# Performance work log

Hardware: AMD Instinct MI355X
Metric: run time of the kernel (lower is better)

Reference implementation:

```python
import jax, jax.numpy as jnp
import numpy as np

N_NODES = 100000
N_EDGES = 1600000
D_IN = 64
D_OUT = 64
K_ORDERS = 4  # K+1 Chebyshev orders (K=3)


def setup_inputs() -> dict:
    key = jax.random.key(0)
    k1, k2, k3, k4, k5 = jax.random.split(key, 5)
    x = jax.random.normal(k1, (N_NODES, D_IN), dtype=jnp.float32)
    edge_index = jax.random.randint(k2, (2, N_EDGES), 0, N_NODES, dtype=jnp.int64)
    edge_attr = jax.random.uniform(k3, (N_EDGES,), dtype=jnp.float32)
    weight = jax.random.normal(k4, (K_ORDERS, D_IN, D_OUT), dtype=jnp.float32) * 0.05
    bias = jax.random.normal(k5, (D_OUT,), dtype=jnp.float32) * 0.05
    return {"x": x, "edge_index": edge_index, "edge_attr": edge_attr,
            "weight": weight, "bias": bias}


def reference(x, edge_index, edge_attr, weight, bias):
    n = x.shape[0]
    row, col = edge_index[0], edge_index[1]
    # degree = number of edges per destination node (row)
    deg = jax.ops.segment_sum(jnp.ones_like(edge_attr), row, num_segments=n)
    dinv = jnp.where(deg > 0, deg ** -0.5, 0.0)
    # negative normalized adjacency acting as rescaled Laplacian
    lap = -dinv[row] * edge_attr * dinv[col]  # [E]

    def spmm(h):  # out[row] += lap * h[col]
        return jax.ops.segment_sum(lap[:, None] * h[col], row, num_segments=n)

    k_orders = weight.shape[0]
    tx0 = x
    out = tx0 @ weight[0]
    tx1 = spmm(tx0)
    out = out + tx1 @ weight[1]
    for k in range(2, k_orders):  # small fixed K, fine to unroll
        tx2 = 2.0 * spmm(tx1) - tx0
        out = out + tx2 @ weight[k]
        tx0, tx1 = tx1, tx2
    return out + bias
```

## Files before the change

kernel.cpp:

```cpp
#include <hip/hip_runtime.h>

#define D 64
#define BLK 256

#define NBSHIFT 9
#define NODES_PER_BKT 512
#define TA 4096

typedef unsigned int uint32;
typedef __attribute__((ext_vector_type(8))) short bf16x8;
typedef __attribute__((ext_vector_type(4))) float f32x4;

__device__ inline uint32 f2bf_u(float f) {
    uint32 u = __float_as_uint(f);
    u += 0x7FFFu + ((u >> 16) & 1u);
    return u >> 16;
}

__global__ void cvt_kernel(const float* __restrict__ x, uint2* __restrict__ xb, int n4) {
    int i = blockIdx.x * BLK + threadIdx.x;
    if (i < n4) {
        float4 v = ((const float4*)x)[i];
        uint2 pack;
        pack.x = f2bf_u(v.x) | (f2bf_u(v.y) << 16);
        pack.y = f2bf_u(v.z) | (f2bf_u(v.w) << 16);
        xb[i] = pack;
    }
}

__global__ void wf_kernel(const float* __restrict__ W, uint4* __restrict__ Wf) {
    int tid = blockIdx.x * 256 + threadIdx.x;
    int l = tid & 63;
    int g = tid >> 6;
    int kh = g & 1;
    int t = (g >> 1) & 3;
    int w = g >> 3;
    int n = t * 16 + (l & 15);
    int kbase = kh * 32 + (l >> 4) * 8;
    uint32 pk[4];
    #pragma unroll
    for (int i = 0; i < 4; ++i) {
        uint32 b0 = f2bf_u(W[(size_t)w * 4096 + (size_t)(kbase + 2 * i) * 64 + n]);
        uint32 b1 = f2bf_u(W[(size_t)w * 4096 + (size_t)(kbase + 2 * i + 1) * 64 + n]);
        pk[i] = b0 | (b1 << 16);
    }
    Wf[tid] = make_uint4(pk[0], pk[1], pk[2], pk[3]);
}

__global__ void hist_kernel(const int* __restrict__ row, uint32* __restrict__ bcount, int E) {
    __shared__ uint32 h[256];
    int tid = threadIdx.x;
    h[tid] = 0;
    __syncthreads();
    int base = blockIdx.x * TA;
    int end = min(base + TA, E);
    for (int e = base + tid; e < end; e += 256)
        atomicAdd(&h[(uint32)row[e] >> NBSHIFT], 1u);
    __syncthreads();
    if (h[tid]) atomicAdd(&bcount[tid], h[tid]);
}

__global__ void scan256_kernel(const uint32* __restrict__ bcount, uint32* __restrict__ gcursor,
                               uint32* __restrict__ bbase, int E) {
    __shared__ uint32 s[256];
    int tid = threadIdx.x;
    uint32 v = bcount[tid];
    s[tid] = v;
    __syncthreads();
    for (int off = 1; off < 256; off <<= 1) {
        uint32 t = (tid >= off) ? s[tid - off] : 0u;
        __syncthreads();
        s[tid] += t;
        __syncthreads();
    }
    uint32 excl = s[tid] - v;
    gcursor[tid] = excl;
    bbase[tid] = excl;
    if (tid == 255) bbase[256] = (uint32)E;
}

__global__ void binA_kernel(const int* __restrict__ row, const int* __restrict__ col,
                            const float* __restrict__ attr,
                            uint32* __restrict__ gcursor, int2* __restrict__ binned, int E) {
    __shared__ uint32 hist[256], baseg[256], lstart[256], lcur[256];
    __shared__ int2 stage[TA];
    __shared__ unsigned char sbkt[TA];
    int tid = threadIdx.x;
    int tile = blockIdx.x * TA;
    hist[tid] = 0;
    __syncthreads();

    uint32 px[16], py[16], bk[16];
    #pragma unroll
    for (int k = 0; k < 16; ++k) {
        int e = tile + k * 256 + tid;
        bk[k] = 0xFFFFFFFFu;
        if (e < E) {
            int r = row[e], c = col[e];
            uint32 b = (uint32)r >> NBSHIFT;
            bk[k] = b;
            px[k] = ((uint32)(r & (NODES_PER_BKT - 1)) << 17) | (uint32)c;
            py[k] = __float_as_uint(attr[e]);
            atomicAdd(&hist[b], 1u);
        }
    }
    __syncthreads();
    lcur[tid] = hist[tid];
    __syncthreads();
    for (int off = 1; off < 256; off <<= 1) {
        uint32 t = (tid >= off) ? lcur[tid - off] : 0u;
        __syncthreads();
        lcur[tid] += t;
        __syncthreads();
    }
    lstart[tid] = lcur[tid] - hist[tid];
    if (hist[tid] > 0) baseg[tid] = atomicAdd(&gcursor[tid], hist[tid]);
    lcur[tid] = lstart[tid];
    __syncthreads();
    #pragma unroll
    for (int k = 0; k < 16; ++k) {
        if (bk[k] != 0xFFFFFFFFu) {
            uint32 pos = atomicAdd(&lcur[bk[k]], 1u);
            stage[pos] = make_int2((int)px[k], (int)py[k]);
            sbkt[pos] = (unsigned char)bk[k];
        }
    }
    __syncthreads();
    int cnt = min(TA, E - tile);
    for (int i = tid; i < cnt; i += 256) {
        uint32 b = sbkt[i];
        uint32 dst = baseg[b] + (uint32)i - lstart[b];
        binned[dst] = stage[i];
    }
}

__global__ void binBdeg_kernel(const int2* __restrict__ binned, const uint32* __restrict__ bbase,
                               uint32* __restrict__ rowptr, float* __restrict__ dinv,
                               int N, int E) {
    __shared__ uint32 cnt[NODES_PER_BKT];
    __shared__ uint32 ps[256];
    int b = blockIdx.x;
    int tid = threadIdx.x;
    cnt[tid] = 0;
    cnt[tid + 256] = 0;
    __syncthreads();
    uint32 start = bbase[b], end = bbase[b + 1];
    for (uint32 i = start + tid; i < end; i += 256)
        atomicAdd(&cnt[(uint32)binned[i].x >> 17], 1u);
    __syncthreads();
    uint32 c0 = cnt[2 * tid], c1 = cnt[2 * tid + 1];
    ps[tid] = c0 + c1;
    __syncthreads();
    for (int off = 1; off < 256; off <<= 1) {
        uint32 t = (tid >= off) ? ps[tid - off] : 0u;
        __syncthreads();
        ps[tid] += t;
        __syncthreads();
    }
    uint32 pexcl = ps[tid] - (c0 + c1);
    int base = b << NBSHIFT;
    int n0 = base + 2 * tid, n1 = n0 + 1;
    if (n0 < N) {
        rowptr[n0] = start + pexcl;
        dinv[n0] = c0 ? rsqrtf((float)c0) : 0.0f;
    }
    if (n1 < N) {
        rowptr[n1] = start + pexcl + c0;
        dinv[n1] = c1 ? rsqrtf((float)c1) : 0.0f;
    }
    if (b == gridDim.x - 1 && tid == 0) rowptr[N] = (uint32)E;
}

__global__ void binBsort_kernel(const int2* __restrict__ binned, const uint32* __restrict__ bbase,
                                const uint32* __restrict__ rowptr, const float* __restrict__ dinv,
                                int2* __restrict__ pairs, int N) {
    __shared__ uint32 lcur[NODES_PER_BKT];
    __shared__ float ldin[NODES_PER_BKT];
    int b = blockIdx.x;
    int tid = threadIdx.x;
    int base = b << NBSHIFT;
    uint32 start = bbase[b], end = bbase[b + 1];
    for (int t = tid; t < NODES_PER_BKT; t += 256) {
        int node = base + t;
        lcur[t] = (node < N) ? (rowptr[node] - start) : 0u;
        ldin[t] = (node < N) ? dinv[node] : 0.0f;
    }
    __syncthreads();
    for (uint32 i = start + tid; i < end; i += 256) {
        int2 rec = binned[i];
        uint32 x = (uint32)rec.x;
        uint32 rl = x >> 17;
        uint32 c = x & 0x1FFFFu;
        float lap = -ldin[rl] * __int_as_float(rec.y) * dinv[c];
        uint32 pos = atomicAdd(&lcur[rl], 1u);
        pairs[start + pos] = make_int2((int)(c << 7), __float_as_int(lap));
    }
}

__global__ void spmm8_kernel(const uint32* __restrict__ rowptr, const int2* __restrict__ pairs,
                             const char* __restrict__ hb, const uint4* __restrict__ prev,
                             uint4* __restrict__ out, float scale, int N) {
    int n = blockIdx.x * 4 + (threadIdx.x >> 6);
    if (n >= N) return;
    int lane = threadIdx.x & 63;
    int q = lane >> 3;
    int sub = lane & 7;
    int off = sub * 16;
    uint32 j = rowptr[n];
    uint32 end = rowptr[n + 1];
    float a[8];
    #pragma unroll
    for (int i = 0; i < 8; ++i) a[i] = 0.0f;

    for (; j + 16 <= end; j += 16) {
        int2 m0 = pairs[j + q];
        int2 m1 = pairs[j + 8 + q];
        uint4 h0 = *(const uint4*)(hb + (uint32)m0.x + off);
        uint4 h1 = *(const uint4*)(hb + (uint32)m1.x + off);
        float l0 = __int_as_float(m0.y);
        float l1 = __int_as_float(m1.y);
        a[0] += l0 * __uint_as_float(h0.x << 16);
        a[1] += l0 * __uint_as_float(h0.x & 0xFFFF0000u);
        a[2] += l0 * __uint_as_float(h0.y << 16);
        a[3] += l0 * __uint_as_float(h0.y & 0xFFFF0000u);
        a[4] += l0 * __uint_as_float(h0.z << 16);
        a[5] += l0 * __uint_as_float(h0.z & 0xFFFF0000u);
        a[6] += l0 * __uint_as_float(h0.w << 16);
        a[7] += l0 * __uint_as_float(h0.w & 0xFFFF0000u);
        a[0] += l1 * __uint_as_float(h1.x << 16);
        a[1] += l1 * __uint_as_float(h1.x & 0xFFFF0000u);
        a[2] += l1 * __uint_as_float(h1.y << 16);
        a[3] += l1 * __uint_as_float(h1.y & 0xFFFF0000u);
        a[4] += l1 * __uint_as_float(h1.z << 16);
        a[5] += l1 * __uint_as_float(h1.z & 0xFFFF0000u);
        a[6] += l1 * __uint_as_float(h1.w << 16);
        a[7] += l1 * __uint_as_float(h1.w & 0xFFFF0000u);
    }
    for (; j < end; j += 8) {
        uint32 idx = j + q;
        bool act = idx < end;
        uint32 ci = act ? idx : (end - 1);
        int2 m = pairs[ci];
        float l = act ? __int_as_float(m.y) : 0.0f;
        uint4 h0 = *(const uint4*)(hb + (uint32)m.x + off);
        a[0] += l * __uint_as_float(h0.x << 16);
        a[1] += l * __uint_as_float(h0.x & 0xFFFF0000u);
        a[2] += l * __uint_as_float(h0.y << 16);
        a[3] += l * __uint_as_float(h0.y & 0xFFFF0000u);
        a[4] += l * __uint_as_float(h0.z << 16);
        a[5] += l * __uint_as_float(h0.z & 0xFFFF0000u);
        a[6] += l * __uint_as_float(h0.w << 16);
        a[7] += l * __uint_as_float(h0.w & 0xFFFF0000u);
    }
    #pragma unroll
    for (int i = 0; i < 8; ++i) {
        a[i] += __shfl_xor(a[i], 8);
        a[i] += __shfl_xor(a[i], 16);
        a[i] += __shfl_xor(a[i], 32);
    }

    if (q == 0) {
        float r[8];
        #pragma unroll
        for (int i = 0; i < 8; ++i) r[i] = scale * a[i];
        size_t slot = (size_t)n * 8 + sub;
        if (prev) {
            uint4 pv = prev[slot];
            r[0] -= __uint_as_float(pv.x << 16);
            r[1] -= __uint_as_float(pv.x & 0xFFFF0000u);
            r[2] -= __uint_as_float(pv.y << 16);
            r[3] -= __uint_as_float(pv.y & 0xFFFF0000u);
            r[4] -= __uint_as_float(pv.z << 16);
            r[5] -= __uint_as_float(pv.z & 0xFFFF0000u);
            r[6] -= __uint_as_float(pv.w << 16);
            r[7] -= __uint_as_float(pv.w & 0xFFFF0000u);
        }
        uint4 pack;
        pack.x = f2bf_u(r[0]) | (f2bf_u(r[1]) << 16);
        pack.y = f2bf_u(r[2]) | (f2bf_u(r[3]) << 16);
        pack.z = f2bf_u(r[4]) | (f2bf_u(r[5]) << 16);
        pack.w = f2bf_u(r[6]) | (f2bf_u(r[7]) << 16);
        out[slot] = pack;
    }
}

__global__ void gemm_mfma(const uint4* __restrict__ h0, const uint4* __restrict__ h1,
                          const uint4* __restrict__ h2, const uint4* __restrict__ h3,
                          const uint4* __restrict__ Wf, const float* __restrict__ bias,
                          float* __restrict__ out, int N) {
    int tid = threadIdx.x;
    int wave = tid >> 6;
    int lane = tid & 63;
    int quad = lane >> 4;
    int lo = lane & 15;
    int m0 = blockIdx.x * 64 + wave * 16;
    int mrow = m0 + lo;
    int mclamp = min(mrow, N - 1);

    f32x4 acc[4] = {{0.f,0.f,0.f,0.f},{0.f,0.f,0.f,0.f},{0.f,0.f,0.f,0.f},{0.f,0.f,0.f,0.f}};
    const uint4* hs[4] = { h0, h1, h2, h3 };
    #pragma unroll
    for (int w = 0; w < 4; ++w) {
        union { uint4 u; bf16x8 v; } a0, a1;
        a0.u = hs[w][(size_t)mclamp * 8 + quad];
        a1.u = hs[w][(size_t)mclamp * 8 + 4 + quad];
        #pragma unroll
        for (int t = 0; t < 4; ++t) {
            union { uint4 u; bf16x8 v; } b0, b1;
            b0.u = Wf[(w * 8 + t * 2 + 0) * 64 + lane];
            b1.u = Wf[(w * 8 + t * 2 + 1) * 64 + lane];
            acc[t] = __builtin_amdgcn_mfma_f32_16x16x32_bf16(a0.v, b0.v, acc[t], 0, 0, 0);
            acc[t] = __builtin_amdgcn_mfma_f32_16x16x32_bf16(a1.v, b1.v, acc[t], 0, 0, 0);
        }
    }
    #pragma unroll
    for (int t = 0; t < 4; ++t) {
        int col = t * 16 + lo;
        float bv = bias[col];
        #pragma unroll
        for (int r = 0; r < 4; ++r) {
            int rowi = m0 + quad * 4 + r;
            if (rowi < N) out[(size_t)rowi * 64 + col] = acc[t][r] + bv;
        }
    }
}

extern "C" void kernel_launch(void* const* d_in, const int* in_sizes, int n_in,
                              void* d_out, int out_size, void* d_ws, size_t ws_size,
                              hipStream_t stream) {
    const float* x    = (const float*)d_in[0];
    const int*   ei   = (const int*)d_in[1];
    const float* attr = (const float*)d_in[2];
    const float* W    = (const float*)d_in[3];
    const float* bias = (const float*)d_in[4];
    float* out = (float*)d_out;

    const int N = in_sizes[0] / D;
    const int E = in_sizes[1] / 2;
    const int* row = ei;
    const int* col = ei + E;
    const int NB = (N + NODES_PER_BKT - 1) >> NBSHIFT;

    char* p = (char*)d_ws;
    int2*     pairs   = (int2*)p;                p += (size_t)E * 8;
    uint2*    xb      = (uint2*)p;               p += (size_t)N * D * 2;
    uint2*    T1      = (uint2*)p;               p += (size_t)N * D * 2;
    uint2*    T2      = (uint2*)p;               p += (size_t)N * D * 2;
    uint2*    T3      = (uint2*)p;               p += (size_t)N * D * 2;
    uint4*    Wf      = (uint4*)p;               p += 2048 * 16;
    uint32*   rowptr  = (uint32*)p;              p += (size_t)(N + 1) * 4;
    uint32*   bcount  = (uint32*)p;              p += 256 * 4;
    uint32*   gcursor = (uint32*)p;              p += 256 * 4;
    uint32*   bbase   = (uint32*)p;              p += 257 * 4;
    float*    dinv    = (float*)p;
    int2*     binned  = (int2*)T3;

    const int gSp = (N + 3) / 4;
    const int gGm = (N + 63) / 64;
    const int gTile = (E + TA - 1) / TA;
    const int gCvt = ((N * D / 4) + BLK - 1) / BLK;

    hipMemsetAsync(bcount, 0, 256 * 4, stream);
    cvt_kernel<<<gCvt, BLK, 0, stream>>>(x, xb, N * D / 4);
    wf_kernel<<<8, 256, 0, stream>>>(W, Wf);
    hist_kernel<<<gTile, 256, 0, stream>>>(row, bcount, E);
    scan256_kernel<<<1, 256, 0, stream>>>(bcount, gcursor, bbase, E);
    binA_kernel<<<gTile, 256, 0, stream>>>(row, col, attr, gcursor, binned, E);
    binBdeg_kernel<<<NB, 256, 0, stream>>>(binned, bbase, rowptr, dinv, N, E);
    binBsort_kernel<<<NB, 256, 0, stream>>>(binned, bbase, rowptr, dinv, pairs, N);

    spmm8_kernel<<<gSp, BLK, 0, stream>>>(rowptr, pairs, (const char*)xb, nullptr, (uint4*)T1, 1.0f, N);
    spmm8_kernel<<<gSp, BLK, 0, stream>>>(rowptr, pairs, (const char*)T1, (const uint4*)xb, (uint4*)T2, 2.0f, N);
    spmm8_kernel<<<gSp, BLK, 0, stream>>>(rowptr, pairs, (const char*)T2, (const uint4*)T1, (uint4*)T3, 2.0f, N);
    gemm_mfma<<<gGm, BLK, 0, stream>>>((const uint4*)xb, (const uint4*)T1, (const uint4*)T2,
                                       (const uint4*)T3, Wf, bias, out, N);
}
```

Baseline: 313.8 us.

## Process two rows per wave in SpMM with interleaved prefetched gathers

The SpMM kernel now assigns two consecutive destination rows to each wavefront. It issues the first 32 edges' index and feature loads for both rows before doing any FMAs, which raises memory-level parallelism and hides gather latency, and it prefetches the previous-order term early. Row bounds are made wave-uniform with readfirstlane and tails are handled with masked loads instead of a separate loop. The trade-offs are higher register pressure from two accumulator sets and more buffered loads, which could lower occupancy, plus half as many waves in the grid.

Result: faster. 291.6 us (-7.1%).

```diff
diff --git a/kernel.cpp b/kernel.cpp
--- a/kernel.cpp
+++ b/kernel.cpp
@@ -197,75 +197,121 @@
     }
 }
 
-__global__ void spmm8_kernel(const uint32* __restrict__ rowptr, const int2* __restrict__ pairs,
-                             const char* __restrict__ hb, const uint4* __restrict__ prev,
-                             uint4* __restrict__ out, float scale, int N) {
-    int n = blockIdx.x * 4 + (threadIdx.x >> 6);
-    if (n >= N) return;
+#define LOAD16(J, END, ESAFE, M0, M1, H0, H1)                          \
+    {                                                                  \
+        uint32 i0_ = (J) + q, i1_ = (J) + 8 + q;                       \
+        uint32 c0_ = (i0_ < (END)) ? i0_ : (ESAFE);                    \
+        uint32 c1_ = (i1_ < (END)) ? i1_ : (ESAFE);                    \
+        M0 = pairs[c0_];                                               \
+        M1 = pairs[c1_];                                               \
+        H0 = *(const uint4*)(hb + (uint32)M0.x + off);                 \
+        H1 = *(const uint4*)(hb + (uint32)M1.x + off);                 \
+    }
+
+#define FMA16(J, END, M0, M1, H0, H1, A)                               \
+    {                                                                  \
+        uint32 i0_ = (J) + q, i1_ = (J) + 8 + q;                       \
+        float l0_ = (i0_ < (END)) ? __int_as_float(M0.y) : 0.0f;       \
+        float l1_ = (i1_ < (END)) ? __int_as_float(M1.y) : 0.0f;       \
+        A[0] += l0_ * __uint_as_float(H0.x << 16);                     \
+        A[1] += l0_ * __uint_as_float(H0.x & 0xFFFF0000u);             \
+        A[2] += l0_ * __uint_as_float(H0.y << 16);                     \
+        A[3] += l0_ * __uint_as_float(H0.y & 0xFFFF0000u);             \
+        A[4] += l0_ * __uint_as_float(H0.z << 16);                     \
+        A[5] += l0_ * __uint_as_float(H0.z & 0xFFFF0000u);             \
+        A[6] += l0_ * __uint_as_float(H0.w << 16);                     \
+        A[7] += l0_ * __uint_as_float(H0.w & 0xFFFF0000u);             \
+        A[0] += l1_ * __uint_as_float(H1.x << 16);                     \
+        A[1] += l1_ * __uint_as_float(H1.x & 0xFFFF0000u);             \
+        A[2] += l1_ * __uint_as_float(H1.y << 16);                     \
+        A[3] += l1_ * __uint_as_float(H1.y & 0xFFFF0000u);             \
+        A[4] += l1_ * __uint_as_float(H1.z << 16);                     \
+        A[5] += l1_ * __uint_as_float(H1.z & 0xFFFF0000u);             \
+        A[6] += l1_ * __uint_as_float(H1.w << 16);                     \
+        A[7] += l1_ * __uint_as_float(H1.w & 0xFFFF0000u);             \
+    }
+
+__global__ void spmm2r_kernel(const uint32* __restrict__ rowptr, const int2* __restrict__ pairs,
+                              const char* __restrict__ hb, const uint4* __restrict__ prev,
+                              uint4* __restrict__ out, float scale, int N) {
+    int wid = blockIdx.x * 4 + (threadIdx.x >> 6);
+    int nA = wid * 2;
+    if (nA >= N) return;
     int lane = threadIdx.x & 63;
     int q = lane >> 3;
     int sub = lane & 7;
     int off = sub * 16;
-    uint32 j = rowptr[n];
-    uint32 end = rowptr[n + 1];
-    float a[8];
-    #pragma unroll
-    for (int i = 0; i < 8; ++i) a[i] = 0.0f;
-
-    for (; j + 16 <= end; j += 16) {
-        int2 m0 = pairs[j + q];
-        int2 m1 = pairs[j + 8 + q];
-        uint4 h0 = *(const uint4*)(hb + (uint32)m0.x + off);
-        uint4 h1 = *(const uint4*)(hb + (uint32)m1.x + off);
-        float l0 = __int_as_float(m0.y);
-        float l1 = __int_as_float(m1.y);
-        a[0] += l0 * __uint_as_float(h0.x << 16);
-        a[1] += l0 * __uint_as_float(h0.x & 0xFFFF0000u);
-        a[2] += l0 * __uint_as_float(h0.y << 16);
-        a[3] += l0 * __uint_as_float(h0.y & 0xFFFF0000u);
-        a[4] += l0 * __uint_as_float(h0.z << 16);
-        a[5] += l0 * __uint_as_float(h0.z & 0xFFFF0000u);
-        a[6] += l0 * __uint_as_float(h0.w << 16);
-        a[7] += l0 * __uint_as_float(h0.w & 0xFFFF0000u);
-        a[0] += l1 * __uint_as_float(h1.x << 16);
-        a[1] += l1 * __uint_as_float(h1.x & 0xFFFF0000u);
-        a[2] += l1 * __uint_as_float(h1.y << 16);
-        a[3] += l1 * __uint_as_float(h1.y & 0xFFFF0000u);
-        a[4] += l1 * __uint_as_float(h1.z << 16);
-        a[5] += l1 * __uint_as_float(h1.z & 0xFFFF0000u);
-        a[6] += l1 * __uint_as_float(h1.w << 16);
-        a[7] += l1 * __uint_as_float(h1.w & 0xFFFF0000u);
-    }
-    for (; j < end; j += 8) {
-        uint32 idx = j + q;
-        bool act = idx < end;
-        uint32 ci = act ? idx : (end - 1);
-        int2 m = pairs[ci];
-        float l = act ? __int_as_float(m.y) : 0.0f;
-        uint4 h0 = *(const uint4*)(hb + (uint32)m.x + off);
-        a[0] += l * __uint_as_float(h0.x << 16);
-        a[1] += l * __uint_as_float(h0.x & 0xFFFF0000u);
-        a[2] += l * __uint_as_float(h0.y << 16);
-        a[3] += l * __uint_as_float(h0.y & 0xFFFF0000u);
-        a[4] += l * __uint_as_float(h0.z << 16);
-        a[5] += l * __uint_as_float(h0.z & 0xFFFF0000u);
-        a[6] += l * __uint_as_float(h0.w << 16);
-        a[7] += l * __uint_as_float(h0.w & 0xFFFF0000u);
-    }
+    bool hasB = (nA + 1 < N);
+
+    uint2 rpA = *(const uint2*)(rowptr + nA);
+    uint32 eBr = hasB ? rowptr[nA + 2] : rpA.y;
+    uint32 jA   = __builtin_amdgcn_readfirstlane(rpA.x);
+    uint32 endA = __builtin_amdgcn_readfirstlane(rpA.y);
+    uint32 jB   = endA;
+    uint32 endB = __builtin_amdgcn_readfirstlane(eBr);
+    uint32 esA = (endA > jA) ? endA - 1 : 0u;
+    uint32 esB = (endB > jB) ? endB - 1 : 0u;
+
+    int nq = nA + (q & 1);
+    uint4 pv = make_uint4(0u, 0u, 0u, 0u);
+    if (prev && q < 2 && nq < N) pv = prev[(size_t)nq * 8 + sub];
+
+    float aA[8], aB[8];
+    #pragma unroll
+    for (int i = 0; i < 8; ++i) { aA[i] = 0.0f; aB[i] = 0.0f; }
+
+    int2 mA0, mA1, mA2, mA3, mB0, mB1, mB2, mB3;
+    uint4 hA0, hA1, hA2, hA3, hB0, hB1, hB2, hB3;
+
+    bool dA = (jA + 16 < endA);
+    bool dB = (jB + 16 < endB);
+
+    LOAD16(jA, endA, esA, mA0, mA1, hA0, hA1);
+    LOAD16(jB, endB, esB, mB0, mB1, hB0, hB1);
+    if (dA) LOAD16(jA + 16, endA, esA, mA2, mA3, hA2, hA3);
+    if (dB) LOAD16(jB + 16, endB, esB, mB2, mB3, hB2, hB3);
+    FMA16(jA, endA, mA0, mA1, hA0, hA1, aA);
+    FMA16(jB, endB, mB0, mB1, hB0, hB1, aB);
+    if (dA) FMA16(jA + 16, endA, mA2, mA3, hA2, hA3, aA);
+    if (dB) FMA16(jB + 16, endB, mB2, mB3, hB2, hB3, aB);
+    jA += 32;
+    jB += 32;
+
+    while (jA < endA) {
+        LOAD16(jA, endA, esA, mA0, mA1, hA0, hA1);
+        FMA16(jA, endA, mA0, mA1, hA0, hA1, aA);
+        if (jA + 16 < endA) {
+            LOAD16(jA + 16, endA, esA, mA2, mA3, hA2, hA3);
+            FMA16(jA + 16, endA, mA2, mA3, hA2, hA3, aA);
+        }
+        jA += 32;
+    }
+    while (jB < endB) {
+        LOAD16(jB, endB, esB, mB0, mB1, hB0, hB1);
+        FMA16(jB, endB, mB0, mB1, hB0, hB1, aB);
+        if (jB + 16 < endB) {
+            LOAD16(jB + 16, endB, esB, mB2, mB3, hB2, hB3);
+            FMA16(jB + 16, endB, mB2, mB3, hB2, hB3, aB);
+        }
+        jB += 32;
+    }
+
     #pragma unroll
     for (int i = 0; i < 8; ++i) {
-        a[i] += __shfl_xor(a[i], 8);
-        a[i] += __shfl_xor(a[i], 16);
-        a[i] += __shfl_xor(a[i], 32);
-    }
-
-    if (q == 0) {
+        aA[i] += __shfl_xor(aA[i], 8);
+        aA[i] += __shfl_xor(aA[i], 16);
+        aA[i] += __shfl_xor(aA[i], 32);
+        aB[i] += __shfl_xor(aB[i], 8);
+        aB[i] += __shfl_xor(aB[i], 16);
+        aB[i] += __shfl_xor(aB[i], 32);
+    }
+
+    if (q < 2 && nq < N) {
+        bool isB = (q == 1);
         float r[8];
         #pragma unroll
-        for (int i = 0; i < 8; ++i) r[i] = scale * a[i];
-        size_t slot = (size_t)n * 8 + sub;
+        for (int i = 0; i < 8; ++i) r[i] = scale * (isB ? aB[i] : aA[i]);
         if (prev) {
-            uint4 pv = prev[slot];
             r[0] -= __uint_as_float(pv.x << 16);
             r[1] -= __uint_as_float(pv.x & 0xFFFF0000u);
             r[2] -= __uint_as_float(pv.y << 16);
@@ -280,7 +326,7 @@
         pack.y = f2bf_u(r[2]) | (f2bf_u(r[3]) << 16);
         pack.z = f2bf_u(r[4]) | (f2bf_u(r[5]) << 16);
         pack.w = f2bf_u(r[6]) | (f2bf_u(r[7]) << 16);
-        out[slot] = pack;
+        out[(size_t)nq * 8 + sub] = pack;
     }
 }
 
@@ -355,7 +401,7 @@
     float*    dinv    = (float*)p;
     int2*     binned  = (int2*)T3;
 
-    const int gSp = (N + 3) / 4;
+    const int gSp = (N + 7) / 8;
     const int gGm = (N + 63) / 64;
     const int gTile = (E + TA - 1) / TA;
     const int gCvt = ((N * D / 4) + BLK - 1) / BLK;
@@ -369,9 +415,9 @@
     binBdeg_kernel<<<NB, 256, 0, stream>>>(binned, bbase, rowptr, dinv, N, E);
     binBsort_kernel<<<NB, 256, 0, stream>>>(binned, bbase, rowptr, dinv, pairs, N);
 
-    spmm8_kernel<<<gSp, BLK, 0, stream>>>(rowptr, pairs, (const char*)xb, nullptr, (uint4*)T1, 1.0f, N);
-    spmm8_kernel<<<gSp, BLK, 0, stream>>>(rowptr, pairs, (const char*)T1, (const uint4*)xb, (uint4*)T2, 2.0f, N);
-    spmm8_kernel<<<gSp, BLK, 0, stream>>>(rowptr, pairs, (const char*)T2, (const uint4*)T1, (uint4*)T3, 2.0f, N);
+    spmm2r_kernel<<<gSp, BLK, 0, stream>>>(rowptr, pairs, (const char*)xb, nullptr, (uint4*)T1, 1.0f, N);
+    spmm2r_kernel<<<gSp, BLK, 0, stream>>>(rowptr, pairs, (const char*)T1, (const uint4*)xb, (uint4*)T2, 2.0f, N);
+    spmm2r_kernel<<<gSp, BLK, 0, stream>>>(rowptr, pairs, (const char*)T2, (const uint4*)T1, (uint4*)T3, 2.0f, N);
     gemm_mfma<<<gGm, BLK, 0, stream>>>((const uint4*)xb, (const uint4*)T1, (const uint4*)T2,
                                        (const uint4*)T3, Wf, bias, out, N);
 }
```

## Process four rows per wavefront in SpMM with batched gather loads

Applied to the files above, without the earlier changes.

The SpMM kernel now assigns four consecutive rows to each wavefront instead of one. It issues the first 32 edges of all four rows' gathers up front before any FMAs, which raises memory-level parallelism for the typical degree of about 16. Row pointers are loaded as one vector and made wave-uniform, and the prev-term load is hoisted ahead of the gathers. In exchange it uses four accumulator sets, which costs more registers and may lower occupancy, and the grid shrinks by four times.

After: 314.4 us. About the same (+0.2%).

```diff
diff --git a/kernel.cpp b/kernel.cpp
--- a/kernel.cpp
+++ b/kernel.cpp
@@ -197,75 +197,160 @@
     }
 }
 
-__global__ void spmm8_kernel(const uint32* __restrict__ rowptr, const int2* __restrict__ pairs,
-                             const char* __restrict__ hb, const uint4* __restrict__ prev,
-                             uint4* __restrict__ out, float scale, int N) {
-    int n = blockIdx.x * 4 + (threadIdx.x >> 6);
-    if (n >= N) return;
+#define LOADQ(J, END, ESAFE, L0, L1, H0, H1)                           \
+    {                                                                  \
+        uint32 i0_ = (J) + q, i1_ = (J) + 8 + q;                       \
+        uint32 c0_ = (i0_ < (END)) ? i0_ : (ESAFE);                    \
+        uint32 c1_ = (i1_ < (END)) ? i1_ : (ESAFE);                    \
+        int2 m0_ = pairs[c0_];                                         \
+        int2 m1_ = pairs[c1_];                                         \
+        H0 = *(const uint4*)(hb + (uint32)m0_.x + off);                \
+        H1 = *(const uint4*)(hb + (uint32)m1_.x + off);                \
+        L0 = (i0_ < (END)) ? __int_as_float(m0_.y) : 0.0f;             \
+        L1 = (i1_ < (END)) ? __int_as_float(m1_.y) : 0.0f;             \
+    }
+
+#define FMAQ(L0, L1, H0, H1, A)                                        \
+    {                                                                  \
+        A[0] += L0 * __uint_as_float(H0.x << 16);                      \
+        A[1] += L0 * __uint_as_float(H0.x & 0xFFFF0000u);              \
+        A[2] += L0 * __uint_as_float(H0.y << 16);                      \
+        A[3] += L0 * __uint_as_float(H0.y & 0xFFFF0000u);              \
+        A[4] += L0 * __uint_as_float(H0.z << 16);                      \
+        A[5] += L0 * __uint_as_float(H0.z & 0xFFFF0000u);              \
+        A[6] += L0 * __uint_as_float(H0.w << 16);                      \
+        A[7] += L0 * __uint_as_float(H0.w & 0xFFFF0000u);              \
+        A[0] += L1 * __uint_as_float(H1.x << 16);                      \
+        A[1] += L1 * __uint_as_float(H1.x & 0xFFFF0000u);              \
+        A[2] += L1 * __uint_as_float(H1.y << 16);                      \
+        A[3] += L1 * __uint_as_float(H1.y & 0xFFFF0000u);              \
+        A[4] += L1 * __uint_as_float(H1.z << 16);                      \
+        A[5] += L1 * __uint_as_float(H1.z & 0xFFFF0000u);              \
+        A[6] += L1 * __uint_as_float(H1.w << 16);                      \
+        A[7] += L1 * __uint_as_float(H1.w & 0xFFFF0000u);              \
+    }
+
+__global__ void spmm4r_kernel(const uint32* __restrict__ rowptr, const int2* __restrict__ pairs,
+                              const char* __restrict__ hb, const uint4* __restrict__ prev,
+                              uint4* __restrict__ out, float scale, int N) {
+    int wid = blockIdx.x * 4 + (threadIdx.x >> 6);
+    int nA = wid * 4;
+    if (nA >= N) return;
     int lane = threadIdx.x & 63;
     int q = lane >> 3;
     int sub = lane & 7;
     int off = sub * 16;
-    uint32 j = rowptr[n];
-    uint32 end = rowptr[n + 1];
-    float a[8];
-    #pragma unroll
-    for (int i = 0; i < 8; ++i) a[i] = 0.0f;
-
-    for (; j + 16 <= end; j += 16) {
-        int2 m0 = pairs[j + q];
-        int2 m1 = pairs[j + 8 + q];
-        uint4 h0 = *(const uint4*)(hb + (uint32)m0.x + off);
-        uint4 h1 = *(const uint4*)(hb + (uint32)m1.x + off);
-        float l0 = __int_as_float(m0.y);
-        float l1 = __int_as_float(m1.y);
-        a[0] += l0 * __uint_as_float(h0.x << 16);
-        a[1] += l0 * __uint_as_float(h0.x & 0xFFFF0000u);
-        a[2] += l0 * __uint_as_float(h0.y << 16);
-        a[3] += l0 * __uint_as_float(h0.y & 0xFFFF0000u);
-        a[4] += l0 * __uint_as_float(h0.z << 16);
-        a[5] += l0 * __uint_as_float(h0.z & 0xFFFF0000u);
-        a[6] += l0 * __uint_as_float(h0.w << 16);
-        a[7] += l0 * __uint_as_float(h0.w & 0xFFFF0000u);
-        a[0] += l1 * __uint_as_float(h1.x << 16);
-        a[1] += l1 * __uint_as_float(h1.x & 0xFFFF0000u);
-        a[2] += l1 * __uint_as_float(h1.y << 16);
-        a[3] += l1 * __uint_as_float(h1.y & 0xFFFF0000u);
-        a[4] += l1 * __uint_as_float(h1.z << 16);
-        a[5] += l1 * __uint_as_float(h1.z & 0xFFFF0000u);
-        a[6] += l1 * __uint_as_float(h1.w << 16);
-        a[7] += l1 * __uint_as_float(h1.w & 0xFFFF0000u);
-    }
-    for (; j < end; j += 8) {
-        uint32 idx = j + q;
-        bool act = idx < end;
-        uint32 ci = act ? idx : (end - 1);
-        int2 m = pairs[ci];
-        float l = act ? __int_as_float(m.y) : 0.0f;
-        uint4 h0 = *(const uint4*)(hb + (uint32)m.x + off);
-        a[0] += l * __uint_as_float(h0.x << 16);
-        a[1] += l * __uint_as_float(h0.x & 0xFFFF0000u);
-        a[2] += l * __uint_as_float(h0.y << 16);
-        a[3] += l * __uint_as_float(h0.y & 0xFFFF0000u);
-        a[4] += l * __uint_as_float(h0.z << 16);
-        a[5] += l * __uint_as_float(h0.z & 0xFFFF0000u);
-        a[6] += l * __uint_as_float(h0.w << 16);
-        a[7] += l * __uint_as_float(h0.w & 0xFFFF0000u);
-    }
+
+    uint32 r0, r1, r2, r3, r4;
+    if (nA + 4 <= N) {
+        uint4 rp = *(const uint4*)(rowptr + nA);
+        r0 = rp.x; r1 = rp.y; r2 = rp.z; r3 = rp.w;
+        r4 = rowptr[nA + 4];
+    } else {
+        r0 = rowptr[nA];
+        r1 = rowptr[min(nA + 1, N)];
+        r2 = rowptr[min(nA + 2, N)];
+        r3 = rowptr[min(nA + 3, N)];
+        r4 = rowptr[N];
+    }
+    uint32 j0 = __builtin_amdgcn_readfirstlane(r0);
+    uint32 e0 = __builtin_amdgcn_readfirstlane(r1);
+    uint32 j1 = e0, e1 = __builtin_amdgcn_readfirstlane(r2);
+    uint32 j2 = e1, e2 = __builtin_amdgcn_readfirstlane(r3);
+    uint32 j3 = e2, e3 = __builtin_amdgcn_readfirstlane(r4);
+    uint32 es0 = (e0 > j0) ? e0 - 1 : 0u;
+    uint32 es1 = (e1 > j1) ? e1 - 1 : 0u;
+    uint32 es2 = (e2 > j2) ? e2 - 1 : 0u;
+    uint32 es3 = (e3 > j3) ? e3 - 1 : 0u;
+
+    int nq = nA + (q & 3);
+    uint4 pv = make_uint4(0u, 0u, 0u, 0u);
+    if (prev && q < 4 && nq < N) pv = prev[(size_t)nq * 8 + sub];
+
+    float a0[8], a1[8], a2[8], a3[8];
+    #pragma unroll
+    for (int i = 0; i < 8; ++i) { a0[i] = 0.0f; a1[i] = 0.0f; a2[i] = 0.0f; a3[i] = 0.0f; }
+
+    float lA0, lA1, lA2, lA3, lB0, lB1, lB2, lB3;
+    float lC0, lC1, lC2, lC3, lD0, lD1, lD2, lD3;
+    uint4 hA0, hA1, hA2, hA3, hB0, hB1, hB2, hB3;
+    uint4 hC0, hC1, hC2, hC3, hD0, hD1, hD2, hD3;
+
+    bool d0 = (j0 + 16 < e0);
+    bool d1 = (j1 + 16 < e1);
+    bool d2 = (j2 + 16 < e2);
+    bool d3 = (j3 + 16 < e3);
+
+    LOADQ(j0, e0, es0, lA0, lA1, hA0, hA1);
+    LOADQ(j1, e1, es1, lB0, lB1, hB0, hB1);
+    LOADQ(j2, e2, es2, lC0, lC1, hC0, hC1);
+    LOADQ(j3, e3, es3, lD0, lD1, hD0, hD1);
+    if (d0) LOADQ(j0 + 16, e0, es0, lA2, lA3, hA2, hA3);
+    if (d1) LOADQ(j1 + 16, e1, es1, lB2, lB3, hB2, hB3);
+    if (d2) LOADQ(j2 + 16, e2, es2, lC2, lC3, hC2, hC3);
+    if (d3) LOADQ(j3 + 16, e3, es3, lD2, lD3, hD2, hD3);
+    FMAQ(lA0, lA1, hA0, hA1, a0);
+    FMAQ(lB0, lB1, hB0, hB1, a1);
+    FMAQ(lC0, lC1, hC0, hC1, a2);
+    FMAQ(lD0, lD1, hD0, hD1, a3);
+    if (d0) FMAQ(lA2, lA3, hA2, hA3, a0);
+    if (d1) FMAQ(lB2, lB3, hB2, hB3, a1);
+    if (d2) FMAQ(lC2, lC3, hC2, hC3, a2);
+    if (d3) FMAQ(lD2, lD3, hD2, hD3, a3);
+    j0 += 32; j1 += 32; j2 += 32; j3 += 32;
+
+    while (j0 < e0) {
+        LOADQ(j0, e0, es0, lA0, lA1, hA0, hA1);
+        FMAQ(lA0, lA1, hA0, hA1, a0);
+        if (j0 + 16 < e0) { LOADQ(j0 + 16, e0, es0, lA2, lA3, hA2, hA3); FMAQ(lA2, lA3, hA2, hA3, a0); }
+        j0 += 32;
+    }
+    while (j1 < e1) {
+        LOADQ(j1, e1, es1, lB0, lB1, hB0, hB1);
+        FMAQ(lB0, lB1, hB0, hB1, a1);
+        if (j1 + 16 < e1) { LOADQ(j1 + 16, e1, es1, lB2, lB3, hB2, hB3); FMAQ(lB2, lB3, hB2, hB3, a1); }
+        j1 += 32;
+    }
+    while (j2 < e2) {
+        LOADQ(j2, e2, es2, lC0, lC1, hC0, hC1);
+        FMAQ(lC0, lC1, hC0, hC1, a2);
+        if (j2 + 16 < e2) { LOADQ(j2 + 16, e2, es2, lC2, lC3, hC2, hC3); FMAQ(lC2, lC3, hC2, hC3, a2); }
+        j2 += 32;
+    }
+    while (j3 < e3) {
+        LOADQ(j3, e3, es3, lD0, lD1, hD0, hD1);
+        FMAQ(lD0, lD1, hD0, hD1, a3);
+        if (j3 + 16 < e3) { LOADQ(j3 + 16, e3, es3, lD2, lD3, hD2, hD3); FMAQ(lD2, lD3, hD2, hD3, a3); }
+        j3 += 32;
+    }
+
     #pragma unroll
     for (int i = 0; i < 8; ++i) {
-        a[i] += __shfl_xor(a[i], 8);
-        a[i] += __shfl_xor(a[i], 16);
-        a[i] += __shfl_xor(a[i], 32);
-    }
-
-    if (q == 0) {
+        a0[i] += __shfl_xor(a0[i], 8);
+        a0[i] += __shfl_xor(a0[i], 16);
+        a0[i] += __shfl_xor(a0[i], 32);
+        a1[i] += __shfl_xor(a1[i], 8);
+        a1[i] += __shfl_xor(a1[i], 16);
+        a1[i] += __shfl_xor(a1[i], 32);
+        a2[i] += __shfl_xor(a2[i], 8);
+        a2[i] += __shfl_xor(a2[i], 16);
+        a2[i] += __shfl_xor(a2[i], 32);
+        a3[i] += __shfl_xor(a3[i], 8);
+        a3[i] += __shfl_xor(a3[i], 16);
+        a3[i] += __shfl_xor(a3[i], 32);
+    }
+
+    if (q < 4 && nq < N) {
         float r[8];
         #pragma unroll
-        for (int i = 0; i < 8; ++i) r[i] = scale * a[i];
-        size_t slot = (size_t)n * 8 + sub;
+        for (int i = 0; i < 8; ++i) {
+            float v = a0[i];
+            if (q == 1) v = a1[i];
+            if (q == 2) v = a2[i];
+            if (q == 3) v = a3[i];
+            r[i] = scale * v;
+        }
         if (prev) {
-            uint4 pv = prev[slot];
             r[0] -= __uint_as_float(pv.x << 16);
             r[1] -= __uint_as_float(pv.x & 0xFFFF0000u);
             r[2] -= __uint_as_float(pv.y << 16);
@@ -280,7 +365,7 @@
         pack.y = f2bf_u(r[2]) | (f2bf_u(r[3]) << 16);
         pack.z = f2bf_u(r[4]) | (f2bf_u(r[5]) << 16);
         pack.w = f2bf_u(r[6]) | (f2bf_u(r[7]) << 16);
-        out[slot] = pack;
+        out[(size_t)nq * 8 + sub] = pack;
     }
 }
 
@@ -355,7 +440,7 @@
     float*    dinv    = (float*)p;
     int2*     binned  = (int2*)T3;
 
-    const int gSp = (N + 3) / 4;
+    const int gSp = (N + 15) / 16;
     const int gGm = (N + 63) / 64;
     const int gTile = (E + TA - 1) / TA;
     const int gCvt = ((N * D / 4) + BLK - 1) / BLK;
@@ -369,9 +454,9 @@
     binBdeg_kernel<<<NB, 256, 0, stream>>>(binned, bbase, rowptr, dinv, N, E);
     binBsort_kernel<<<NB, 256, 0, stream>>>(binned, bbase, rowptr, dinv, pairs, N);
 
-    spmm8_kernel<<<gSp, BLK, 0, stream>>>(rowptr, pairs, (const char*)xb, nullptr, (uint4*)T1, 1.0f, N);
-    spmm8_kernel<<<gSp, BLK, 0, stream>>>(rowptr, pairs, (const char*)T1, (const uint4*)xb, (uint4*)T2, 2.0f, N);
-    spmm8_kernel<<<gSp, BLK, 0, stream>>>(rowptr, pairs, (const char*)T2, (const uint4*)T1, (uint4*)T3, 2.0f, N);
+    spmm4r_kernel<<<gSp, BLK, 0, stream>>>(rowptr, pairs, (const char*)xb, nullptr, (uint4*)T1, 1.0f, N);
+    spmm4r_kernel<<<gSp, BLK, 0, stream>>>(rowptr, pairs, (const char*)T1, (const uint4*)xb, (uint4*)T2, 2.0f, N);
+    spmm4r_kernel<<<gSp, BLK, 0, stream>>>(rowptr, pairs, (const char*)T2, (const uint4*)T1, (uint4*)T3, 2.0f, N);
     gemm_mfma<<<gGm, BLK, 0, stream>>>((const uint4*)xb, (const uint4*)T1, (const uint4*)T2,
                                        (const uint4*)T3, Wf, bias, out, N);
 }
```
